# Kernel optimization log

Hardware: AMD Instinct MI355X
Metric: run time of the kernel (lower is better)

Reference implementation:

```python
import jax, jax.numpy as jnp
import numpy as np

EMBED = 256
HEADS = 8
HEAD_DIM = EMBED // HEADS
K = 7          # kernel_size
DIL = 1        # dilation
PAD = DIL * (K - 1) // 2  # 3
B, H, W = 4, 56, 56


def setup_inputs() -> dict:
    key = jax.random.key(0)
    ks = jax.random.split(key, 9)
    d = {"x": jax.random.normal(ks[0], (B, H, W, EMBED), jnp.float32)}
    for i, name in enumerate(["wq", "wk", "wv", "wo"]):
        d[name] = jax.random.normal(ks[1 + i], (EMBED, EMBED), jnp.float32) * 0.02
    for i, name in enumerate(["bq", "bk", "bv", "bo"]):
        d[name] = jax.random.normal(ks[5 + i], (EMBED,), jnp.float32) * 0.02
    return d


def _unfold(t):
    # t: [N, d, H, W] -> [N, d, K*K, H, W]; zero padding (matches F.unfold),
    # so out-of-bounds neighbors contribute logit 0, NOT -inf (faithful to source).
    h, w = t.shape[2], t.shape[3]
    tp = jnp.pad(t, ((0, 0), (0, 0), (PAD, PAD), (PAD, PAD)))
    patches = [tp[:, :, i * DIL:i * DIL + h, j * DIL:j * DIL + w]
               for i in range(K) for j in range(K)]  # fixed K*K=49 offsets
    return jnp.stack(patches, axis=2)


def reference(x, wq, bq, wk, bk, wv, bv, wo, bo):
    b, h, w, c = x.shape
    scale = HEAD_DIM ** -0.5
    q = x @ wq.T + bq
    k = x @ wk.T + bk
    v = x @ wv.T + bv

    def to_nh(t):  # [B,H,W,C] -> [B*heads, head_dim, H, W]
        return t.reshape(b, h, w, HEADS, HEAD_DIM).transpose(0, 3, 4, 1, 2).reshape(b * HEADS, HEAD_DIM, h, w)

    q, k, v = to_nh(q), to_nh(k), to_nh(v)
    k_unf = _unfold(k)  # [N, d, K2, H, W]
    v_unf = _unfold(v)
    logits = jnp.einsum('ndhw,ndkhw->nkhw', q, k_unf) * scale  # [N, K2, H, W]
    attn = jax.nn.softmax(logits, axis=1)
    out = jnp.einsum('nkhw,ndkhw->ndhw', attn, v_unf)  # [N, d, H, W]
    out = out.reshape(b, HEADS, HEAD_DIM, h, w).transpose(0, 3, 4, 1, 2).reshape(b, h, w, c)
    return out @ wo.T + bo
```

## Files before the change

### kernel.cpp

```cpp
#include <hip/hip_runtime.h>

typedef unsigned int u32;
typedef unsigned short u16;
typedef __attribute__((ext_vector_type(8))) short bf16x8;
typedef __attribute__((ext_vector_type(4))) float f32x4;

#define T_TOK 12544
#define EMB   256
#define IMG   56
#define SCALE 0.17677669529663689f
#define HALO  196
#define KSTR  40
#define VTSTR 208
#define PSTR  136

__device__ __forceinline__ u32 bf16_rtne(float f) {
    u32 u = __builtin_bit_cast(u32, f);
    return (u + 0x7fffu + ((u >> 16) & 1u)) >> 16;
}
__device__ __forceinline__ float bf16_to_f(u32 h) { return __builtin_bit_cast(float, h << 16); }

#define GLD16(g, l) __builtin_amdgcn_global_load_lds( \
    (const __attribute__((address_space(1))) u32*)(g), \
    (__attribute__((address_space(3))) u32*)(l), 16, 0, 0)

__global__ __launch_bounds__(256) void convert_kernel(
    const float* __restrict__ x, const float* __restrict__ wq, const float* __restrict__ wk,
    const float* __restrict__ wv, const float* __restrict__ wo,
    u16* __restrict__ xb, u16* __restrict__ bsh,
    u16* __restrict__ boh, u16* __restrict__ bol) {
    const int i = blockIdx.x * 256 + threadIdx.x;
    const int NX4 = T_TOK * EMB / 4;
    if (i < NX4) {
        const float4 f = ((const float4*)x)[i];
        const float vf[4] = {f.x, f.y, f.z, f.w};
        ushort4 hv;
        u16* hp = (u16*)&hv;
        #pragma unroll
        for (int c = 0; c < 4; ++c) hp[c] = (u16)bf16_rtne(vf[c]);
        ((ushort4*)xb)[i] = hv;
    } else {
        const int j = i - NX4;
        const int w = j >> 14, widx = j & 16383;
        const float* src = (w == 0) ? wq : (w == 1) ? wk : (w == 2) ? wv : wo;
        const float4 f = ((const float4*)src)[widx];
        const float vf[4] = {f.x, f.y, f.z, f.w};
        if (w < 3) {
            ushort4 hv;
            u16* hp = (u16*)&hv;
            #pragma unroll
            for (int c = 0; c < 4; ++c) hp[c] = (u16)bf16_rtne(vf[c]);
            ((ushort4*)bsh)[(w << 14) + widx] = hv;
        } else {
            ushort4 hv, lv;
            u16* hp = (u16*)&hv; u16* lp = (u16*)&lv;
            #pragma unroll
            for (int c = 0; c < 4; ++c) {
                const u32 h = bf16_rtne(vf[c]);
                hp[c] = (u16)h;
                lp[c] = (u16)bf16_rtne(vf[c] - bf16_to_f(h));
            }
            ((ushort4*)boh)[widx] = hv;
            ((ushort4*)bol)[widx] = lv;
        }
    }
}

__global__ __launch_bounds__(256) void qkv_mfma(
    const u16* __restrict__ xb, const u16* __restrict__ bsh,
    const float* __restrict__ bq, const float* __restrict__ bk, const float* __restrict__ bv,
    u16* __restrict__ qb, u16* __restrict__ kb, u16* __restrict__ vb) {
    __shared__ __attribute__((aligned(16))) u16 sA[2][64 * 32];
    __shared__ __attribute__((aligned(16))) u16 sB[2][64 * 32];
    const int nBase = blockIdx.x * 64;
    const int mBase = blockIdx.y * 64;
    const int tid = threadIdx.x, wv = tid >> 6, ln = tid & 63;
    const int lrow = ln & 15, lqd = ln >> 4;
    const int rA = tid >> 2, kcA = tid & 3;
    const size_t gA = (size_t)(mBase + rA) * EMB + kcA * 8;
    const size_t gB = (size_t)(nBase + rA) * EMB + kcA * 8;
    const int lA = wv * 64 * 8;

    f32x4 acc[4];
    #pragma unroll
    for (int mi = 0; mi < 4; ++mi) acc[mi] = (f32x4){0.f, 0.f, 0.f, 0.f};

    GLD16(xb  + gA, &sA[0][lA]);
    GLD16(bsh + gB, &sB[0][lA]);

    for (int kt = 0; kt < 8; ++kt) {
        const int b = kt & 1;
        __syncthreads();
        if (kt < 7) {
            const int k0 = (kt + 1) * 32;
            GLD16(xb  + gA + k0, &sA[b ^ 1][lA]);
            GLD16(bsh + gB + k0, &sB[b ^ 1][lA]);
        }
        bf16x8 af[4];
        #pragma unroll
        for (int mi = 0; mi < 4; ++mi)
            af[mi] = *(const bf16x8*)&sA[b][(mi * 16 + lrow) * 32 + lqd * 8];
        const bf16x8 bf = *(const bf16x8*)&sB[b][(wv * 16 + lrow) * 32 + lqd * 8];
        #pragma unroll
        for (int mi = 0; mi < 4; ++mi)
            acc[mi] = __builtin_amdgcn_mfma_f32_16x16x32_bf16(af[mi], bf, acc[mi], 0, 0, 0);
    }

    const int which = nBase >> 8;
    const float* bias = (which == 0) ? bq : (which == 1) ? bk : bv;
    u16* dst = (which == 0) ? qb : (which == 1) ? kb : vb;
    const int c = (nBase & 255) + wv * 16 + lrow;
    const float bz = bias[c];
    #pragma unroll
    for (int mi = 0; mi < 4; ++mi) {
        #pragma unroll
        for (int r = 0; r < 4; ++r) {
            const int row = mBase + mi * 16 + lqd * 4 + r;
            dst[(size_t)row * EMB + c] = (u16)bf16_rtne(acc[mi][r] + bz);
        }
    }
}

__global__ __launch_bounds__(256) void out_mfma(
    const u16* __restrict__ aoh, const u16* __restrict__ aol,
    const u16* __restrict__ boh, const u16* __restrict__ bol,
    const float* __restrict__ bo, float* __restrict__ out) {
    __shared__ __attribute__((aligned(16))) u16 sAh[2][64 * 32];
    __shared__ __attribute__((aligned(16))) u16 sAl[2][64 * 32];
    __shared__ __attribute__((aligned(16))) u16 sBh[2][64 * 32];
    __shared__ __attribute__((aligned(16))) u16 sBl[2][64 * 32];
    const int nBase = blockIdx.x * 64;
    const int mBase = blockIdx.y * 64;
    const int tid = threadIdx.x, wv = tid >> 6, ln = tid & 63;
    const int lrow = ln & 15, lqd = ln >> 4;
    const int rA = tid >> 2, kcA = tid & 3;
    const size_t gA = (size_t)(mBase + rA) * EMB + kcA * 8;
    const size_t gB = (size_t)(nBase + rA) * EMB + kcA * 8;
    const int lA = wv * 64 * 8;

    f32x4 acc[4];
    #pragma unroll
    for (int mi = 0; mi < 4; ++mi) acc[mi] = (f32x4){0.f, 0.f, 0.f, 0.f};

    GLD16(aoh + gA, &sAh[0][lA]);
    GLD16(aol + gA, &sAl[0][lA]);
    GLD16(boh + gB, &sBh[0][lA]);
    GLD16(bol + gB, &sBl[0][lA]);

    for (int kt = 0; kt < 8; ++kt) {
        const int b = kt & 1;
        __syncthreads();
        if (kt < 7) {
            const int k0 = (kt + 1) * 32;
            GLD16(aoh + gA + k0, &sAh[b ^ 1][lA]);
            GLD16(aol + gA + k0, &sAl[b ^ 1][lA]);
            GLD16(boh + gB + k0, &sBh[b ^ 1][lA]);
            GLD16(bol + gB + k0, &sBl[b ^ 1][lA]);
        }
        bf16x8 ah[4], al[4];
        #pragma unroll
        for (int mi = 0; mi < 4; ++mi) {
            ah[mi] = *(const bf16x8*)&sAh[b][(mi * 16 + lrow) * 32 + lqd * 8];
            al[mi] = *(const bf16x8*)&sAl[b][(mi * 16 + lrow) * 32 + lqd * 8];
        }
        const bf16x8 bh = *(const bf16x8*)&sBh[b][(wv * 16 + lrow) * 32 + lqd * 8];
        const bf16x8 bl = *(const bf16x8*)&sBl[b][(wv * 16 + lrow) * 32 + lqd * 8];
        #pragma unroll
        for (int mi = 0; mi < 4; ++mi) {
            acc[mi] = __builtin_amdgcn_mfma_f32_16x16x32_bf16(ah[mi], bh, acc[mi], 0, 0, 0);
            acc[mi] = __builtin_amdgcn_mfma_f32_16x16x32_bf16(al[mi], bh, acc[mi], 0, 0, 0);
            acc[mi] = __builtin_amdgcn_mfma_f32_16x16x32_bf16(ah[mi], bl, acc[mi], 0, 0, 0);
        }
    }

    const int ncol = nBase + wv * 16 + lrow;
    const float bz = bo[ncol];
    #pragma unroll
    for (int mi = 0; mi < 4; ++mi) {
        #pragma unroll
        for (int r = 0; r < 4; ++r) {
            const int row = mBase + mi * 16 + lqd * 4 + r;
            out[(size_t)row * EMB + ncol] = acc[mi][r] + bz;
        }
    }
}

__global__ __launch_bounds__(256, 5) void attn_kernel(
    const u16* __restrict__ qb, const u16* __restrict__ kb, const u16* __restrict__ vb,
    u16* __restrict__ aoh, u16* __restrict__ aol) {
    __shared__ __attribute__((aligned(16))) u16 smem[15360];
    u16* sVT = smem;
    u16* sK  = smem + 6656;
    u16* sP  = smem + 6656;

    const int tid = threadIdx.x;
    const int w = tid >> 6, ln = tid & 63;
    const int lrow = ln & 15, lqd = ln >> 4;
    const int img = blockIdx.z >> 3, head = blockIdx.z & 7;
    const int ty0 = blockIdx.y * 8, tx0 = blockIdx.x * 8;
    const int base8 = (28 * w) & ~7;

    for (int i = tid; i < 1664; i += 256) {
        const int mv = (i >= 832) ? 1 : 0;
        const int ii = i - 832 * mv;
        const int p = ii >> 2, c = ii & 3;
        const int pyh = p / 14, pxh = p - pyh * 14;
        const int gy = ty0 - 3 + pyh, gx = tx0 - 3 + pxh;
        const bool ok = (p < HALO) & ((unsigned)gy < 56u) & ((unsigned)gx < 56u);
        if (!mv) {
            u16* dstk = sK + p * KSTR + c * 8;
            if (ok) {
                const size_t tt = ((size_t)img * IMG + gy) * IMG + gx;
                *(uint4*)dstk = *(const uint4*)(kb + tt * EMB + head * 32 + c * 8);
            } else {
                *(uint4*)dstk = (uint4){0u, 0u, 0u, 0u};
            }
        } else {
            u16* dv = sVT + (c * 8) * VTSTR + p;
            if (ok) {
                const size_t tt = ((size_t)img * IMG + gy) * IMG + gx;
                const uint4 u = *(const uint4*)(vb + tt * EMB + head * 32 + c * 8);
                dv[0 * VTSTR] = (u16)(u.x & 0xffffu);
                dv[1 * VTSTR] = (u16)(u.x >> 16);
                dv[2 * VTSTR] = (u16)(u.y & 0xffffu);
                dv[3 * VTSTR] = (u16)(u.y >> 16);
                dv[4 * VTSTR] = (u16)(u.z & 0xffffu);
                dv[5 * VTSTR] = (u16)(u.z >> 16);
                dv[6 * VTSTR] = (u16)(u.w & 0xffffu);
                dv[7 * VTSTR] = (u16)(u.w >> 16);
            } else {
                #pragma unroll
                for (int j = 0; j < 8; ++j) dv[j * VTSTR] = 0;
            }
        }
    }

    const int mpix = w * 16 + lrow;
    const int qpy = mpix >> 3, qpx = mpix & 7;
    const size_t qtok = ((size_t)img * IMG + ty0 + qpy) * IMG + tx0 + qpx;
    const bf16x8 aq = *(const bf16x8*)&qb[qtok * EMB + head * 32 + lqd * 8];
    __syncthreads();

    f32x4 ct[8];
    #pragma unroll
    for (int t = 0; t < 8; ++t) ct[t] = (f32x4){0.f, 0.f, 0.f, 0.f};
    #pragma unroll
    for (int t = 0; t < 8; ++t) {
        const bf16x8 bk = *(const bf16x8*)&sK[(base8 + t * 16 + lrow) * KSTR + lqd * 8];
        ct[t] = __builtin_amdgcn_mfma_f32_16x16x32_bf16(aq, bk, ct[t], 0, 0, 0);
    }

    int pys[4], pxs[4];
    #pragma unroll
    for (int r = 0; r < 4; ++r) {
        const int row = lqd * 4 + r;
        pys[r] = 2 * w + (row >> 3);
        pxs[r] = row & 7;
    }
    float mr4[4] = {-1e30f, -1e30f, -1e30f, -1e30f};
    #pragma unroll
    for (int t = 0; t < 8; ++t) {
        const int col = base8 + t * 16 + lrow;
        const int hy = col / 14, hx = col - 14 * hy;
        const bool okc = (col < HALO);
        #pragma unroll
        for (int r = 0; r < 4; ++r) {
            const bool ok = ((unsigned)(hy - pys[r]) < 7u) &
                            ((unsigned)(hx - pxs[r]) < 7u) & okc;
            const float lv = ok ? ct[t][r] * SCALE : -1e30f;
            ct[t][r] = lv;
            mr4[r] = fmaxf(mr4[r], lv);
        }
    }
    #pragma unroll
    for (int r = 0; r < 4; ++r) {
        float m = mr4[r];
        m = fmaxf(m, __shfl_xor(m, 1));
        m = fmaxf(m, __shfl_xor(m, 2));
        m = fmaxf(m, __shfl_xor(m, 4));
        m = fmaxf(m, __shfl_xor(m, 8));
        mr4[r] = m;
    }
    float sr4[4] = {0.f, 0.f, 0.f, 0.f};
    #pragma unroll
    for (int t = 0; t < 8; ++t)
        #pragma unroll
        for (int r = 0; r < 4; ++r) {
            const float e = __expf(ct[t][r] - mr4[r]);
            ct[t][r] = e;
            sr4[r] += e;
        }
    #pragma unroll
    for (int r = 0; r < 4; ++r) {
        float s = sr4[r];
        s += __shfl_xor(s, 1);
        s += __shfl_xor(s, 2);
        s += __shfl_xor(s, 4);
        s += __shfl_xor(s, 8);
        sr4[r] = 1.0f / s;
    }

    __syncthreads();

    u16* sPw = sP + w * 16 * PSTR;
    #pragma unroll
    for (int t = 0; t < 8; ++t)
        #pragma unroll
        for (int r = 0; r < 4; ++r)
            sPw[(lqd * 4 + r) * PSTR + t * 16 + lrow] = (u16)bf16_rtne(ct[t][r]);

    f32x4 o0 = (f32x4){0.f, 0.f, 0.f, 0.f};
    f32x4 o1 = (f32x4){0.f, 0.f, 0.f, 0.f};
    #pragma unroll
    for (int ks = 0; ks < 4; ++ks) {
        const bf16x8 ap  = *(const bf16x8*)&sPw[lrow * PSTR + ks * 32 + lqd * 8];
        const bf16x8 bv0 = *(const bf16x8*)&sVT[lrow * VTSTR + base8 + ks * 32 + lqd * 8];
        const bf16x8 bv1 = *(const bf16x8*)&sVT[(16 + lrow) * VTSTR + base8 + ks * 32 + lqd * 8];
        o0 = __builtin_amdgcn_mfma_f32_16x16x32_bf16(ap, bv0, o0, 0, 0, 0);
        o1 = __builtin_amdgcn_mfma_f32_16x16x32_bf16(ap, bv1, o1, 0, 0, 0);
    }

    #pragma unroll
    for (int r = 0; r < 4; ++r) {
        const int row = lqd * 4 + r;
        const int opy = 2 * w + (row >> 3), opx = row & 7;
        const size_t ot = ((size_t)img * IMG + ty0 + opy) * IMG + tx0 + opx;
        const float inv = sr4[r];
        const float v0 = o0[r] * inv;
        const float v1 = o1[r] * inv;
        const size_t base = ot * EMB + head * 32;
        const u32 h0 = bf16_rtne(v0);
        aoh[base + lrow] = (u16)h0;
        aol[base + lrow] = (u16)bf16_rtne(v0 - bf16_to_f(h0));
        const u32 h1 = bf16_rtne(v1);
        aoh[base + 16 + lrow] = (u16)h1;
        aol[base + 16 + lrow] = (u16)bf16_rtne(v1 - bf16_to_f(h1));
    }
}

extern "C" void kernel_launch(void* const* d_in, const int* in_sizes, int n_in,
                              void* d_out, int out_size, void* d_ws, size_t ws_size,
                              hipStream_t stream) {
    const float* x  = (const float*)d_in[0];
    const float* wq = (const float*)d_in[1];
    const float* wk = (const float*)d_in[2];
    const float* wv = (const float*)d_in[3];
    const float* wo = (const float*)d_in[4];
    const float* bq = (const float*)d_in[5];
    const float* bk = (const float*)d_in[6];
    const float* bv = (const float*)d_in[7];
    const float* bo = (const float*)d_in[8];
    float* out = (float*)d_out;

    char* ws = (char*)d_ws;
    u16* xb  = (u16*)(ws);
    u16* qb  = (u16*)(ws +  6422528);
    u16* kb  = (u16*)(ws + 12845056);
    u16* vb  = (u16*)(ws + 19267584);
    u16* aoh = (u16*)(ws + 25690112);
    u16* aol = (u16*)(ws + 32112640);
    u16* bsh = (u16*)(ws + 38535168);
    u16* boh = (u16*)(ws + 38928384);
    u16* bol = (u16*)(ws + 39059456);

    convert_kernel<<<3392, 256, 0, stream>>>(x, wq, wk, wv, wo, xb, bsh, boh, bol);
    qkv_mfma<<<dim3(12, 196), 256, 0, stream>>>(xb, bsh, bq, bk, bv, qb, kb, vb);
    attn_kernel<<<dim3(7, 7, 32), 256, 0, stream>>>(qb, kb, vb, aoh, aol);
    out_mfma<<<dim3(4, 196), 256, 0, stream>>>(aoh, aol, boh, bol, bo, out);
}
```

Measured before the change: 130.2 us.

## Enlarge QKV GEMM tiles, store Q/K/V head-major, use exp2 softmax

The QKV projection moves from 64x64 to 128x128 block tiles, with each wave computing a 64x64 sub-tile. This raises operand reuse per LDS load and cuts the block count. Q/K/V are now written in a head-major layout [head][token][32], so the attention kernel's halo gathers read contiguous 64-byte rows per token instead of strided slices. The softmax folds log2(e) into the scale and uses exp2f. Trade-offs: fewer blocks mean less occupancy, and the epilogue stores are still scattered 2-byte writes.

After: 130.7 us. Within noise of the previous version (+0.4%).

```diff
diff --git a/kernel.cpp b/kernel.cpp
--- a/kernel.cpp
+++ b/kernel.cpp
@@ -8,7 +8,7 @@
 #define T_TOK 12544
 #define EMB   256
 #define IMG   56
-#define SCALE 0.17677669529663689f
+#define SCALE2 0.25503486f
 #define HALO  196
 #define KSTR  40
 #define VTSTR 208
@@ -70,53 +70,70 @@
     const u16* __restrict__ xb, const u16* __restrict__ bsh,
     const float* __restrict__ bq, const float* __restrict__ bk, const float* __restrict__ bv,
     u16* __restrict__ qb, u16* __restrict__ kb, u16* __restrict__ vb) {
-    __shared__ __attribute__((aligned(16))) u16 sA[2][64 * 32];
-    __shared__ __attribute__((aligned(16))) u16 sB[2][64 * 32];
-    const int nBase = blockIdx.x * 64;
-    const int mBase = blockIdx.y * 64;
+    __shared__ __attribute__((aligned(16))) u16 sA[2][128 * 32];
+    __shared__ __attribute__((aligned(16))) u16 sB[2][128 * 32];
+    const int nBase = blockIdx.x * 128;
+    const int mBase = blockIdx.y * 128;
     const int tid = threadIdx.x, wv = tid >> 6, ln = tid & 63;
     const int lrow = ln & 15, lqd = ln >> 4;
+    const int wr = wv >> 1, wc = wv & 1;
     const int rA = tid >> 2, kcA = tid & 3;
     const size_t gA = (size_t)(mBase + rA) * EMB + kcA * 8;
     const size_t gB = (size_t)(nBase + rA) * EMB + kcA * 8;
-    const int lA = wv * 64 * 8;
-
-    f32x4 acc[4];
-    #pragma unroll
-    for (int mi = 0; mi < 4; ++mi) acc[mi] = (f32x4){0.f, 0.f, 0.f, 0.f};
-
-    GLD16(xb  + gA, &sA[0][lA]);
-    GLD16(bsh + gB, &sB[0][lA]);
+    const int lA = wv * 512;
+
+    f32x4 acc[4][4];
+    #pragma unroll
+    for (int mi = 0; mi < 4; ++mi)
+        #pragma unroll
+        for (int ni = 0; ni < 4; ++ni) acc[mi][ni] = (f32x4){0.f, 0.f, 0.f, 0.f};
+
+    GLD16(xb  + gA,            &sA[0][lA]);
+    GLD16(xb  + gA + 64 * EMB, &sA[0][2048 + lA]);
+    GLD16(bsh + gB,            &sB[0][lA]);
+    GLD16(bsh + gB + 64 * EMB, &sB[0][2048 + lA]);
 
     for (int kt = 0; kt < 8; ++kt) {
         const int b = kt & 1;
         __syncthreads();
         if (kt < 7) {
             const int k0 = (kt + 1) * 32;
-            GLD16(xb  + gA + k0, &sA[b ^ 1][lA]);
-            GLD16(bsh + gB + k0, &sB[b ^ 1][lA]);
-        }
-        bf16x8 af[4];
+            GLD16(xb  + gA + k0,            &sA[b ^ 1][lA]);
+            GLD16(xb  + gA + k0 + 64 * EMB, &sA[b ^ 1][2048 + lA]);
+            GLD16(bsh + gB + k0,            &sB[b ^ 1][lA]);
+            GLD16(bsh + gB + k0 + 64 * EMB, &sB[b ^ 1][2048 + lA]);
+        }
+        bf16x8 af[4], bfr[4];
         #pragma unroll
         for (int mi = 0; mi < 4; ++mi)
-            af[mi] = *(const bf16x8*)&sA[b][(mi * 16 + lrow) * 32 + lqd * 8];
-        const bf16x8 bf = *(const bf16x8*)&sB[b][(wv * 16 + lrow) * 32 + lqd * 8];
+            af[mi] = *(const bf16x8*)&sA[b][(wr * 64 + mi * 16 + lrow) * 32 + lqd * 8];
+        #pragma unroll
+        for (int ni = 0; ni < 4; ++ni)
+            bfr[ni] = *(const bf16x8*)&sB[b][(wc * 64 + ni * 16 + lrow) * 32 + lqd * 8];
         #pragma unroll
         for (int mi = 0; mi < 4; ++mi)
-            acc[mi] = __builtin_amdgcn_mfma_f32_16x16x32_bf16(af[mi], bf, acc[mi], 0, 0, 0);
+            #pragma unroll
+            for (int ni = 0; ni < 4; ++ni)
+                acc[mi][ni] = __builtin_amdgcn_mfma_f32_16x16x32_bf16(af[mi], bfr[ni], acc[mi][ni], 0, 0, 0);
     }
 
     const int which = nBase >> 8;
     const float* bias = (which == 0) ? bq : (which == 1) ? bk : bv;
     u16* dst = (which == 0) ? qb : (which == 1) ? kb : vb;
-    const int c = (nBase & 255) + wv * 16 + lrow;
-    const float bz = bias[c];
-    #pragma unroll
-    for (int mi = 0; mi < 4; ++mi) {
-        #pragma unroll
-        for (int r = 0; r < 4; ++r) {
-            const int row = mBase + mi * 16 + lqd * 4 + r;
-            dst[(size_t)row * EMB + c] = (u16)bf16_rtne(acc[mi][r] + bz);
+    #pragma unroll
+    for (int ni = 0; ni < 4; ++ni) {
+        const int cg = (nBase & 255) + wc * 64 + ni * 16;
+        const int head = cg >> 5;
+        const int d = (cg & 31) + lrow;
+        const float bz = bias[cg + lrow];
+        u16* dh = dst + (size_t)head * T_TOK * 32;
+        #pragma unroll
+        for (int mi = 0; mi < 4; ++mi) {
+            #pragma unroll
+            for (int r = 0; r < 4; ++r) {
+                const int row = mBase + wr * 64 + mi * 16 + lqd * 4 + r;
+                dh[(size_t)row * 32 + d] = (u16)bf16_rtne(acc[mi][ni][r] + bz);
+            }
         }
     }
 }
@@ -200,6 +217,10 @@
     const int ty0 = blockIdx.y * 8, tx0 = blockIdx.x * 8;
     const int base8 = (28 * w) & ~7;
 
+    const u16* kbh = kb + (size_t)head * (T_TOK * 32);
+    const u16* vbh = vb + (size_t)head * (T_TOK * 32);
+    const u16* qbh = qb + (size_t)head * (T_TOK * 32);
+
     for (int i = tid; i < 1664; i += 256) {
         const int mv = (i >= 832) ? 1 : 0;
         const int ii = i - 832 * mv;
@@ -207,19 +228,18 @@
         const int pyh = p / 14, pxh = p - pyh * 14;
         const int gy = ty0 - 3 + pyh, gx = tx0 - 3 + pxh;
         const bool ok = (p < HALO) & ((unsigned)gy < 56u) & ((unsigned)gx < 56u);
+        const size_t tt = (size_t)((img * IMG + gy) * IMG + gx) * 32;
         if (!mv) {
             u16* dstk = sK + p * KSTR + c * 8;
             if (ok) {
-                const size_t tt = ((size_t)img * IMG + gy) * IMG + gx;
-                *(uint4*)dstk = *(const uint4*)(kb + tt * EMB + head * 32 + c * 8);
+                *(uint4*)dstk = *(const uint4*)(kbh + tt + c * 8);
             } else {
                 *(uint4*)dstk = (uint4){0u, 0u, 0u, 0u};
             }
         } else {
             u16* dv = sVT + (c * 8) * VTSTR + p;
             if (ok) {
-                const size_t tt = ((size_t)img * IMG + gy) * IMG + gx;
-                const uint4 u = *(const uint4*)(vb + tt * EMB + head * 32 + c * 8);
+                const uint4 u = *(const uint4*)(vbh + tt + c * 8);
                 dv[0 * VTSTR] = (u16)(u.x & 0xffffu);
                 dv[1 * VTSTR] = (u16)(u.x >> 16);
                 dv[2 * VTSTR] = (u16)(u.y & 0xffffu);
@@ -238,7 +258,7 @@
     const int mpix = w * 16 + lrow;
     const int qpy = mpix >> 3, qpx = mpix & 7;
     const size_t qtok = ((size_t)img * IMG + ty0 + qpy) * IMG + tx0 + qpx;
-    const bf16x8 aq = *(const bf16x8*)&qb[qtok * EMB + head * 32 + lqd * 8];
+    const bf16x8 aq = *(const bf16x8*)&qbh[qtok * 32 + lqd * 8];
     __syncthreads();
 
     f32x4 ct[8];
@@ -267,7 +287,7 @@
         for (int r = 0; r < 4; ++r) {
             const bool ok = ((unsigned)(hy - pys[r]) < 7u) &
                             ((unsigned)(hx - pxs[r]) < 7u) & okc;
-            const float lv = ok ? ct[t][r] * SCALE : -1e30f;
+            const float lv = ok ? ct[t][r] * SCALE2 : -1e30f;
             ct[t][r] = lv;
             mr4[r] = fmaxf(mr4[r], lv);
         }
@@ -286,7 +306,7 @@
     for (int t = 0; t < 8; ++t)
         #pragma unroll
         for (int r = 0; r < 4; ++r) {
-            const float e = __expf(ct[t][r] - mr4[r]);
+            const float e = exp2f(ct[t][r] - mr4[r]);
             ct[t][r] = e;
             sr4[r] += e;
         }
@@ -364,7 +384,7 @@
     u16* bol = (u16*)(ws + 39059456);
 
     convert_kernel<<<3392, 256, 0, stream>>>(x, wq, wk, wv, wo, xb, bsh, boh, bol);
-    qkv_mfma<<<dim3(12, 196), 256, 0, stream>>>(xb, bsh, bq, bk, bv, qb, kb, vb);
+    qkv_mfma<<<dim3(6, 98), 256, 0, stream>>>(xb, bsh, bq, bk, bv, qb, kb, vb);
     attn_kernel<<<dim3(7, 7, 32), 256, 0, stream>>>(qb, kb, vb, aoh, aol);
     out_mfma<<<dim3(4, 196), 256, 0, stream>>>(aoh, aol, boh, bol, bo, out);
 }
```
